# Performance work log

Measured on AMD Instinct MI355X. Metric: run time of the kernel, lower is better.

## Reference

```python
import jax, jax.numpy as jnp
import numpy as np

N = 100000      # nodes
E = 800000      # edges (avg degree 8)
F_IN = 512      # num_features
H = 256         # 2 * embedding_size
D_OUT = 128     # embedding_size


def setup_inputs() -> dict:
    key = jax.random.key(0)
    ks = jax.random.split(key, 5)
    x = jax.random.normal(ks[0], (N, F_IN), dtype=jnp.float32)
    edge_index = jax.random.randint(ks[1], (2, E), 0, N, dtype=jnp.int64)
    W1 = jax.random.normal(ks[2], (F_IN, H), dtype=jnp.float32) * (1.0 / np.sqrt(F_IN))
    b1 = jnp.zeros((H,), dtype=jnp.float32)
    W2 = jax.random.normal(ks[3], (H, D_OUT), dtype=jnp.float32) * (1.0 / np.sqrt(H))
    b2 = jnp.zeros((D_OUT,), dtype=jnp.float32)
    return {"x": x, "edge_index": edge_index, "W1": W1, "b1": b1, "W2": W2, "b2": b2}


def _gcn_conv(x, edge_index, W, b):
    # PyG GCNConv: add self-loops, symmetric deg^-1/2 normalization,
    # linear transform, scatter-add aggregation at destination nodes.
    n = x.shape[0]
    loop = jnp.arange(n, dtype=edge_index.dtype)
    src = jnp.concatenate([edge_index[0], loop])  # source j
    dst = jnp.concatenate([edge_index[1], loop])  # target i
    h = x @ W                                      # [N, F_out]
    deg = jax.ops.segment_sum(jnp.ones_like(dst, dtype=h.dtype), dst, num_segments=n)
    dinv = jnp.where(deg > 0, jax.lax.rsqrt(deg), 0.0)
    norm = dinv[src] * dinv[dst]                   # [E + N]
    msg = h[src] * norm[:, None]                   # gather + scale
    out = jax.ops.segment_sum(msg, dst, num_segments=n)
    return out + b


def reference(x, edge_index, W1, b1, W2, b2):
    h = jax.nn.relu(_gcn_conv(x, edge_index, W1, b1))
    # F.dropout with training=False is identity (eval mode)
    return _gcn_conv(h, edge_index, W2, b2)
```

## Files before the change

kernel.cpp:

```cpp
#include <hip/hip_runtime.h>


typedef float   f32x4  __attribute__((ext_vector_type(4)));
typedef float   f32x2  __attribute__((ext_vector_type(2)));
typedef __bf16  bf16x8 __attribute__((ext_vector_type(8)));
typedef __bf16  bf16x4 __attribute__((ext_vector_type(4)));
typedef __bf16  bf16x2 __attribute__((ext_vector_type(2)));

#define NN 100000
#define EE 800000
#define FIN 512
#define HID 256
#define DOUT 128

__global__ void k_count(const int* __restrict__ dst, int E, int* __restrict__ cnt) {
    int e = blockIdx.x * 256 + threadIdx.x;
    if (e < E) atomicAdd(&cnt[dst[e]], 1);
}

__global__ void k_scan1(const int* __restrict__ cnt, int* __restrict__ off,
                        int* __restrict__ sums, int n) {
    __shared__ int s[1024];
    int i = blockIdx.x * 1024 + threadIdx.x;
    int v = (i < n) ? cnt[i] : 0;
    s[threadIdx.x] = v;
    __syncthreads();
    for (int d = 1; d < 1024; d <<= 1) {
        int t = (threadIdx.x >= d) ? s[threadIdx.x - d] : 0;
        __syncthreads();
        s[threadIdx.x] += t;
        __syncthreads();
    }
    if (i < n) off[i] = s[threadIdx.x] - v;
    if (threadIdx.x == 1023) sums[blockIdx.x] = s[1023];
}

__global__ void k_scan2(int* __restrict__ sums, int nb) {
    __shared__ int s[128];
    int t = threadIdx.x;
    int v = (t < nb) ? sums[t] : 0;
    s[t] = v;
    __syncthreads();
    for (int d = 1; d < 128; d <<= 1) {
        int u = (t >= d) ? s[t - d] : 0;
        __syncthreads();
        s[t] += u;
        __syncthreads();
    }
    if (t < nb) sums[t] = s[t] - v;
}

__global__ void k_scan_fix(int* __restrict__ off, const int* __restrict__ sums,
                           const int* __restrict__ cnt, float* __restrict__ dinv, int n) {
    int i = blockIdx.x * 256 + threadIdx.x;
    if (i < n) {
        off[i] += sums[i >> 10];
        dinv[i] = rsqrtf((float)(cnt[i] + 1));
    }
}

__global__ void k_fill(const int* __restrict__ src, const int* __restrict__ dst, int E,
                       const int* __restrict__ off, int* __restrict__ cur,
                       int* __restrict__ csr) {
    int e = blockIdx.x * 256 + threadIdx.x;
    if (e < E) {
        int d = dst[e];
        int p = atomicAdd(&cur[d], 1);
        csr[off[d] + p] = src[e];
    }
}

__global__ void k_prep_w(const float* __restrict__ W1, const float* __restrict__ W2,
                         __bf16* __restrict__ W1t, __bf16* __restrict__ W2t) {
    int id = blockIdx.x * 256 + threadIdx.x;
    if (id < FIN * HID) {
        int k = id >> 8, n = id & 255;
        W1t[n * FIN + k] = (__bf16)W1[id];
    }
    int id2 = id - FIN * HID;
    if (id2 >= 0 && id2 < HID * DOUT) {
        int k = id2 >> 7, n = id2 & 127;
        W2t[n * HID + k] = (__bf16)W2[id2];
    }
}

template <int WAVES_N, bool AF32, int KTOT>
__global__ __launch_bounds__(128 * WAVES_N) void k_gemm(
    const void* __restrict__ Asrc, const __bf16* __restrict__ Bt,
    const float* __restrict__ dinv, __bf16* __restrict__ out, int M) {
    constexpr int BN  = WAVES_N * 64;
    constexpr int LDA = 40;
    __shared__ __bf16 A_lds[128 * LDA];
    __shared__ __bf16 B_lds[BN * LDA];

    const int tid = threadIdx.x;
    const int l = tid & 63, wid = tid >> 6;
    const int wm = wid & 1, wn = wid >> 1;
    const int bm = blockIdx.x;
    const int r15 = l & 15, hi = l >> 4;

    f32x4 acc[4][4] = {};

    for (int kb = 0; kb < KTOT / 32; ++kb) {
        __syncthreads();
        if constexpr (AF32) {
            int row = tid >> 2, seg = tid & 3;
            long rg = (long)bm * 128 + row;
            if (rg >= M) rg = M - 1;
            const float* ap = (const float*)Asrc + rg * (long)KTOT + kb * 32 + seg * 8;
            f32x4 x0 = *(const f32x4*)ap;
            f32x4 x1 = *(const f32x4*)(ap + 4);
            bf16x8 w;
            w[0] = (__bf16)x0[0]; w[1] = (__bf16)x0[1]; w[2] = (__bf16)x0[2]; w[3] = (__bf16)x0[3];
            w[4] = (__bf16)x1[0]; w[5] = (__bf16)x1[1]; w[6] = (__bf16)x1[2]; w[7] = (__bf16)x1[3];
            *(bf16x8*)&A_lds[row * LDA + seg * 8] = w;
        } else {
            int row = tid >> 1, seg = tid & 1;
            long rg = (long)bm * 128 + row;
            if (rg >= M) rg = M - 1;
            const __bf16* ap = (const __bf16*)Asrc + rg * (long)KTOT + kb * 32 + seg * 16;
            bf16x8 u0 = *(const bf16x8*)ap;
            bf16x8 u1 = *(const bf16x8*)(ap + 8);
            *(bf16x8*)&A_lds[row * LDA + seg * 16]     = u0;
            *(bf16x8*)&A_lds[row * LDA + seg * 16 + 8] = u1;
        }
        {
            int n = tid >> 1, seg = tid & 1;
            const __bf16* bp = Bt + (long)n * KTOT + kb * 32 + seg * 16;
            bf16x8 u0 = *(const bf16x8*)bp;
            bf16x8 u1 = *(const bf16x8*)(bp + 8);
            *(bf16x8*)&B_lds[n * LDA + seg * 16]     = u0;
            *(bf16x8*)&B_lds[n * LDA + seg * 16 + 8] = u1;
        }
        __syncthreads();

        bf16x8 af[4], bfr[4];
#pragma unroll
        for (int m = 0; m < 4; m++)
            af[m] = *(const bf16x8*)&A_lds[(wm * 64 + m * 16 + r15) * LDA + hi * 8];
#pragma unroll
        for (int n = 0; n < 4; n++)
            bfr[n] = *(const bf16x8*)&B_lds[(wn * 64 + n * 16 + r15) * LDA + hi * 8];
#pragma unroll
        for (int m = 0; m < 4; m++)
#pragma unroll
            for (int n = 0; n < 4; n++)
                acc[m][n] = __builtin_amdgcn_mfma_f32_16x16x32_bf16(bfr[n], af[m], acc[m][n], 0, 0, 0);
    }

#pragma unroll
    for (int m = 0; m < 4; m++) {
        long rg = (long)bm * 128 + wm * 64 + m * 16 + r15;
        if (rg >= M) continue;
        float di = dinv[rg];
#pragma unroll
        for (int n = 0; n < 4; n++) {
            bf16x4 o;
            o[0] = (__bf16)(acc[m][n][0] * di);
            o[1] = (__bf16)(acc[m][n][1] * di);
            o[2] = (__bf16)(acc[m][n][2] * di);
            o[3] = (__bf16)(acc[m][n][3] * di);
            int c = wn * 64 + n * 16 + hi * 4;
            *(bf16x4*)(out + rg * (long)BN + c) = o;
        }
    }
}

__global__ void k_agg1(const __bf16* __restrict__ g1, const int* __restrict__ csr,
                       const int* __restrict__ off, const int* __restrict__ cnt,
                       const float* __restrict__ dinv, const float* __restrict__ b1,
                       __bf16* __restrict__ z1, int n) {
    int node = blockIdx.x * 4 + (threadIdx.x >> 6);
    if (node >= n) return;
    int l = threadIdx.x & 63;
    bf16x4 v = *(const bf16x4*)(g1 + (size_t)node * HID + l * 4);
    float a0 = (float)v[0], a1 = (float)v[1], a2 = (float)v[2], a3 = (float)v[3];
    int s0 = off[node], e0 = s0 + cnt[node];
    for (int e = s0; e < e0; ++e) {
        int s = csr[e];
        bf16x4 u = *(const bf16x4*)(g1 + (size_t)s * HID + l * 4);
        a0 += (float)u[0]; a1 += (float)u[1]; a2 += (float)u[2]; a3 += (float)u[3];
    }
    float di = dinv[node];
    f32x4 b = *(const f32x4*)(b1 + l * 4);
    bf16x4 o;
    o[0] = (__bf16)fmaxf(a0 * di + b[0], 0.f);
    o[1] = (__bf16)fmaxf(a1 * di + b[1], 0.f);
    o[2] = (__bf16)fmaxf(a2 * di + b[2], 0.f);
    o[3] = (__bf16)fmaxf(a3 * di + b[3], 0.f);
    *(bf16x4*)(z1 + (size_t)node * HID + l * 4) = o;
}

__global__ void k_agg2(const __bf16* __restrict__ g2, const int* __restrict__ csr,
                       const int* __restrict__ off, const int* __restrict__ cnt,
                       const float* __restrict__ dinv, const float* __restrict__ b2,
                       float* __restrict__ out, int n) {
    int node = blockIdx.x * 4 + (threadIdx.x >> 6);
    if (node >= n) return;
    int l = threadIdx.x & 63;
    bf16x2 v = *(const bf16x2*)(g2 + (size_t)node * DOUT + l * 2);
    float a0 = (float)v[0], a1 = (float)v[1];
    int s0 = off[node], e0 = s0 + cnt[node];
    for (int e = s0; e < e0; ++e) {
        int s = csr[e];
        bf16x2 u = *(const bf16x2*)(g2 + (size_t)s * DOUT + l * 2);
        a0 += (float)u[0]; a1 += (float)u[1];
    }
    float di = dinv[node];
    f32x2 b = *(const f32x2*)(b2 + l * 2);
    f32x2 o;
    o[0] = a0 * di + b[0];
    o[1] = a1 * di + b[1];
    *(f32x2*)(out + (size_t)node * DOUT + l * 2) = o;
}

extern "C" void kernel_launch(void* const* d_in, const int* in_sizes, int n_in,
                              void* d_out, int out_size, void* d_ws, size_t ws_size,
                              hipStream_t stream) {
    const float* x  = (const float*)d_in[0];
    const int*   ei = (const int*)d_in[1];
    const float* W1 = (const float*)d_in[2];
    const float* b1 = (const float*)d_in[3];
    const float* W2 = (const float*)d_in[4];
    const float* b2 = (const float*)d_in[5];
    float* out = (float*)d_out;

    const int N = in_sizes[0] / FIN;
    const int E = in_sizes[1] / 2;
    const int* srcA = ei;
    const int* dstA = ei + E;

    uint8_t* w = (uint8_t*)d_ws;
    auto take = [&](size_t bytes) { uint8_t* p = w; w += (bytes + 255) & ~(size_t)255; return p; };
    int*    cnt  = (int*)take((size_t)N * 4);
    int*    cur  = (int*)take((size_t)N * 4);
    int*    off  = (int*)take((size_t)N * 4);
    float*  dinv = (float*)take((size_t)N * 4);
    int*    sums = (int*)take(4096);
    int*    csr  = (int*)take((size_t)E * 4);
    __bf16* W1t  = (__bf16*)take((size_t)FIN * HID * 2);
    __bf16* W2t  = (__bf16*)take((size_t)HID * DOUT * 2);
    __bf16* g1   = (__bf16*)take((size_t)N * HID * 2);
    __bf16* z1   = (__bf16*)take((size_t)N * HID * 2);
    __bf16* g2   = (__bf16*)take((size_t)N * DOUT * 2);

    hipMemsetAsync(cnt, 0, (size_t)N * 4, stream);
    hipMemsetAsync(cur, 0, (size_t)N * 4, stream);
    k_count<<<(E + 255) / 256, 256, 0, stream>>>(dstA, E, cnt);
    int nb = (N + 1023) / 1024;
    k_scan1<<<nb, 1024, 0, stream>>>(cnt, off, sums, N);
    k_scan2<<<1, 128, 0, stream>>>(sums, nb);
    k_scan_fix<<<(N + 255) / 256, 256, 0, stream>>>(off, sums, cnt, dinv, N);
    k_fill<<<(E + 255) / 256, 256, 0, stream>>>(srcA, dstA, E, off, cur, csr);

    k_prep_w<<<(FIN * HID + HID * DOUT + 255) / 256, 256, 0, stream>>>(W1, W2, W1t, W2t);

    const int gm = (N + 127) / 128;

    k_gemm<4, true, FIN><<<gm, 512, 0, stream>>>(x, W1t, dinv, g1, N);
    k_agg1<<<(N + 3) / 4, 256, 0, stream>>>(g1, csr, off, cnt, dinv, b1, z1, N);

    k_gemm<2, false, HID><<<gm, 256, 0, stream>>>(z1, W2t, dinv, g2, N);
    k_agg2<<<(N + 3) / 4, 256, 0, stream>>>(g2, csr, off, cnt, dinv, b2, out, N);
}
```

Measured before the change: 644.9 us.

## Double-buffer GEMM tiles with direct global-to-LDS loads and unroll aggregation gathers

Both GEMMs become double-buffered. The next K-tile is loaded through global_load_lds, the direct global-to-LDS path, while MFMAs run on the current tile. GEMM1 now uses 4 waves, each computing a 64x128 sub-tile, and drops the padded LDS stride. The aggregation kernels unroll the neighbour loop by 4 with two accumulators so more gathers are in flight. The unpadded 32-element LDS rows may cause bank conflicts, and the larger accumulator tile raises register pressure.

```diff
diff --git a/kernel.cpp b/kernel.cpp
--- a/kernel.cpp
+++ b/kernel.cpp
@@ -7,11 +7,14 @@
 typedef __bf16  bf16x4 __attribute__((ext_vector_type(4)));
 typedef __bf16  bf16x2 __attribute__((ext_vector_type(2)));
 
-#define NN 100000
-#define EE 800000
 #define FIN 512
 #define HID 256
 #define DOUT 128
+
+__device__ __forceinline__ void gload16(const void* g, void* l) {
+    __builtin_amdgcn_global_load_lds((const __attribute__((address_space(1))) void*)g,
+                                     (__attribute__((address_space(3))) void*)l, 16, 0, 0);
+}
 
 __global__ void k_count(const int* __restrict__ dst, int E, int* __restrict__ cnt) {
     int e = blockIdx.x * 256 + threadIdx.x;
@@ -84,84 +87,185 @@
     }
 }
 
-template <int WAVES_N, bool AF32, int KTOT>
-__global__ __launch_bounds__(128 * WAVES_N) void k_gemm(
-    const void* __restrict__ Asrc, const __bf16* __restrict__ Bt,
-    const float* __restrict__ dinv, __bf16* __restrict__ out, int M) {
-    constexpr int BN  = WAVES_N * 64;
-    constexpr int LDA = 40;
-    __shared__ __bf16 A_lds[128 * LDA];
-    __shared__ __bf16 B_lds[BN * LDA];
+__global__ __launch_bounds__(256, 2) void k_gemm1(
+    const float* __restrict__ x, const __bf16* __restrict__ Bt,
+    const float* __restrict__ dinv, __bf16* __restrict__ g1, int M) {
+    __shared__ __bf16 Albuf[2][128 * 32];
+    __shared__ __bf16 Blbuf[2][256 * 32];
 
     const int tid = threadIdx.x;
     const int l = tid & 63, wid = tid >> 6;
     const int wm = wid & 1, wn = wid >> 1;
-    const int bm = blockIdx.x;
     const int r15 = l & 15, hi = l >> 4;
-
-    f32x4 acc[4][4] = {};
-
-    for (int kb = 0; kb < KTOT / 32; ++kb) {
-        __syncthreads();
-        if constexpr (AF32) {
-            int row = tid >> 2, seg = tid & 3;
-            long rg = (long)bm * 128 + row;
-            if (rg >= M) rg = M - 1;
-            const float* ap = (const float*)Asrc + rg * (long)KTOT + kb * 32 + seg * 8;
-            f32x4 x0 = *(const f32x4*)ap;
-            f32x4 x1 = *(const f32x4*)(ap + 4);
-            bf16x8 w;
-            w[0] = (__bf16)x0[0]; w[1] = (__bf16)x0[1]; w[2] = (__bf16)x0[2]; w[3] = (__bf16)x0[3];
-            w[4] = (__bf16)x1[0]; w[5] = (__bf16)x1[1]; w[6] = (__bf16)x1[2]; w[7] = (__bf16)x1[3];
-            *(bf16x8*)&A_lds[row * LDA + seg * 8] = w;
-        } else {
-            int row = tid >> 1, seg = tid & 1;
-            long rg = (long)bm * 128 + row;
-            if (rg >= M) rg = M - 1;
-            const __bf16* ap = (const __bf16*)Asrc + rg * (long)KTOT + kb * 32 + seg * 16;
-            bf16x8 u0 = *(const bf16x8*)ap;
-            bf16x8 u1 = *(const bf16x8*)(ap + 8);
-            *(bf16x8*)&A_lds[row * LDA + seg * 16]     = u0;
-            *(bf16x8*)&A_lds[row * LDA + seg * 16 + 8] = u1;
-        }
-        {
-            int n = tid >> 1, seg = tid & 1;
-            const __bf16* bp = Bt + (long)n * KTOT + kb * 32 + seg * 16;
-            bf16x8 u0 = *(const bf16x8*)bp;
-            bf16x8 u1 = *(const bf16x8*)(bp + 8);
-            *(bf16x8*)&B_lds[n * LDA + seg * 16]     = u0;
-            *(bf16x8*)&B_lds[n * LDA + seg * 16 + 8] = u1;
-        }
-        __syncthreads();
-
-        bf16x8 af[4], bfr[4];
-#pragma unroll
-        for (int m = 0; m < 4; m++)
-            af[m] = *(const bf16x8*)&A_lds[(wm * 64 + m * 16 + r15) * LDA + hi * 8];
-#pragma unroll
-        for (int n = 0; n < 4; n++)
-            bfr[n] = *(const bf16x8*)&B_lds[(wn * 64 + n * 16 + r15) * LDA + hi * 8];
-#pragma unroll
-        for (int m = 0; m < 4; m++)
-#pragma unroll
-            for (int n = 0; n < 4; n++)
+    const long bm = blockIdx.x;
+
+    const int arow = tid >> 1, aseg = tid & 1;
+    long ag = bm * 128 + arow;
+    if (ag >= M) ag = M - 1;
+    const float* aptr = x + ag * (long)FIN + aseg * 16;
+    const int aoff = arow * 32 + aseg * 16;
+
+    const int bo0 = wid * 4096;
+
+    f32x4 acc[4][8] = {};
+
+    auto stageB = [&](int kb, int buf) {
+#pragma unroll
+        for (int i = 0; i < 4; ++i) {
+            int ob = bo0 + i * 1024;
+            int o = ob + l * 16;
+            int n = o >> 6, cb = o & 63;
+            const char* src = (const char*)Bt + (long)n * (FIN * 2) + kb * 64 + cb;
+            gload16(src, (char*)&Blbuf[buf][0] + ob);
+        }
+    };
+
+    stageB(0, 0);
+    {
+        const f32x4* p = (const f32x4*)aptr;
+        f32x4 p0 = p[0], p1 = p[1], p2 = p[2], p3 = p[3];
+        bf16x8 w0, w1;
+#pragma unroll
+        for (int j = 0; j < 4; ++j) {
+            w0[j] = (__bf16)p0[j]; w0[j + 4] = (__bf16)p1[j];
+            w1[j] = (__bf16)p2[j]; w1[j + 4] = (__bf16)p3[j];
+        }
+        *(bf16x8*)&Albuf[0][aoff] = w0;
+        *(bf16x8*)&Albuf[0][aoff + 8] = w1;
+    }
+    __syncthreads();
+
+    int cur = 0;
+    constexpr int NT = FIN / 32;
+    for (int kb = 0; kb < NT; ++kb) {
+        const int nxt = cur ^ 1;
+        const bool pf = (kb + 1 < NT);
+        f32x4 p0, p1, p2, p3;
+        if (pf) {
+            stageB(kb + 1, nxt);
+            const f32x4* p = (const f32x4*)(aptr + (kb + 1) * 32);
+            p0 = p[0]; p1 = p[1]; p2 = p[2]; p3 = p[3];
+        }
+
+        bf16x8 af[4], bfr[8];
+#pragma unroll
+        for (int m = 0; m < 4; ++m)
+            af[m] = *(const bf16x8*)&Albuf[cur][(wm * 64 + m * 16 + r15) * 32 + hi * 8];
+#pragma unroll
+        for (int n = 0; n < 8; ++n)
+            bfr[n] = *(const bf16x8*)&Blbuf[cur][(wn * 128 + n * 16 + r15) * 32 + hi * 8];
+#pragma unroll
+        for (int m = 0; m < 4; ++m)
+#pragma unroll
+            for (int n = 0; n < 8; ++n)
                 acc[m][n] = __builtin_amdgcn_mfma_f32_16x16x32_bf16(bfr[n], af[m], acc[m][n], 0, 0, 0);
-    }
-
-#pragma unroll
-    for (int m = 0; m < 4; m++) {
-        long rg = (long)bm * 128 + wm * 64 + m * 16 + r15;
+
+        if (pf) {
+            bf16x8 w0, w1;
+#pragma unroll
+            for (int j = 0; j < 4; ++j) {
+                w0[j] = (__bf16)p0[j]; w0[j + 4] = (__bf16)p1[j];
+                w1[j] = (__bf16)p2[j]; w1[j + 4] = (__bf16)p3[j];
+            }
+            *(bf16x8*)&Albuf[nxt][aoff] = w0;
+            *(bf16x8*)&Albuf[nxt][aoff + 8] = w1;
+        }
+        __syncthreads();
+        cur = nxt;
+    }
+
+#pragma unroll
+    for (int m = 0; m < 4; ++m) {
+        long rg = bm * 128 + wm * 64 + m * 16 + r15;
         if (rg >= M) continue;
         float di = dinv[rg];
 #pragma unroll
-        for (int n = 0; n < 4; n++) {
+        for (int n = 0; n < 8; ++n) {
+            bf16x4 o;
+            o[0] = (__bf16)(acc[m][n][0] * di);
+            o[1] = (__bf16)(acc[m][n][1] * di);
+            o[2] = (__bf16)(acc[m][n][2] * di);
+            o[3] = (__bf16)(acc[m][n][3] * di);
+            int c = wn * 128 + n * 16 + hi * 4;
+            *(bf16x4*)(g1 + rg * (long)HID + c) = o;
+        }
+    }
+}
+
+__global__ __launch_bounds__(256, 3) void k_gemm2(
+    const __bf16* __restrict__ z1, const __bf16* __restrict__ Bt,
+    const float* __restrict__ dinv, __bf16* __restrict__ g2, int M) {
+    __shared__ __bf16 Albuf[2][128 * 32];
+    __shared__ __bf16 Blbuf[2][128 * 32];
+
+    const int tid = threadIdx.x;
+    const int l = tid & 63, wid = tid >> 6;
+    const int wm = wid & 1, wn = wid >> 1;
+    const int r15 = l & 15, hi = l >> 4;
+    const long bm = blockIdx.x;
+
+    f32x4 acc[4][4] = {};
+
+    auto stage = [&](int kb, int buf) {
+#pragma unroll
+        for (int i = 0; i < 2; ++i) {
+            int ob = wid * 2048 + i * 1024;
+            int o = ob + l * 16;
+            long r = bm * 128 + (o >> 6);
+            if (r >= M) r = M - 1;
+            const char* src = (const char*)z1 + r * (HID * 2) + kb * 64 + (o & 63);
+            gload16(src, (char*)&Albuf[buf][0] + ob);
+        }
+#pragma unroll
+        for (int i = 0; i < 2; ++i) {
+            int ob = wid * 2048 + i * 1024;
+            int o = ob + l * 16;
+            int n = o >> 6;
+            const char* src = (const char*)Bt + (long)n * (HID * 2) + kb * 64 + (o & 63);
+            gload16(src, (char*)&Blbuf[buf][0] + ob);
+        }
+    };
+
+    stage(0, 0);
+    __syncthreads();
+
+    int cur = 0;
+    constexpr int NT = HID / 32;
+    for (int kb = 0; kb < NT; ++kb) {
+        const int nxt = cur ^ 1;
+        if (kb + 1 < NT) stage(kb + 1, nxt);
+
+        bf16x8 af[4], bfr[4];
+#pragma unroll
+        for (int m = 0; m < 4; ++m)
+            af[m] = *(const bf16x8*)&Albuf[cur][(wm * 64 + m * 16 + r15) * 32 + hi * 8];
+#pragma unroll
+        for (int n = 0; n < 4; ++n)
+            bfr[n] = *(const bf16x8*)&Blbuf[cur][(wn * 64 + n * 16 + r15) * 32 + hi * 8];
+#pragma unroll
+        for (int m = 0; m < 4; ++m)
+#pragma unroll
+            for (int n = 0; n < 4; ++n)
+                acc[m][n] = __builtin_amdgcn_mfma_f32_16x16x32_bf16(bfr[n], af[m], acc[m][n], 0, 0, 0);
+
+        __syncthreads();
+        cur = nxt;
+    }
+
+#pragma unroll
+    for (int m = 0; m < 4; ++m) {
+        long rg = bm * 128 + wm * 64 + m * 16 + r15;
+        if (rg >= M) continue;
+        float di = dinv[rg];
+#pragma unroll
+        for (int n = 0; n < 4; ++n) {
             bf16x4 o;
             o[0] = (__bf16)(acc[m][n][0] * di);
             o[1] = (__bf16)(acc[m][n][1] * di);
             o[2] = (__bf16)(acc[m][n][2] * di);
             o[3] = (__bf16)(acc[m][n][3] * di);
             int c = wn * 64 + n * 16 + hi * 4;
-            *(bf16x4*)(out + rg * (long)BN + c) = o;
+            *(bf16x4*)(g2 + rg * (long)DOUT + c) = o;
         }
     }
 }
@@ -173,21 +277,34 @@
     int node = blockIdx.x * 4 + (threadIdx.x >> 6);
     if (node >= n) return;
     int l = threadIdx.x & 63;
-    bf16x4 v = *(const bf16x4*)(g1 + (size_t)node * HID + l * 4);
+    const __bf16* base = g1 + (size_t)l * 4;
+    bf16x4 v = *(const bf16x4*)(base + (size_t)node * HID);
     float a0 = (float)v[0], a1 = (float)v[1], a2 = (float)v[2], a3 = (float)v[3];
-    int s0 = off[node], e0 = s0 + cnt[node];
-    for (int e = s0; e < e0; ++e) {
+    float c0 = 0.f, c1 = 0.f, c2 = 0.f, c3 = 0.f;
+    int e = off[node], e0 = e + cnt[node];
+    for (; e + 3 < e0; e += 4) {
+        int sA = csr[e], sB = csr[e + 1], sC = csr[e + 2], sD = csr[e + 3];
+        bf16x4 uA = *(const bf16x4*)(base + (size_t)sA * HID);
+        bf16x4 uB = *(const bf16x4*)(base + (size_t)sB * HID);
+        bf16x4 uC = *(const bf16x4*)(base + (size_t)sC * HID);
+        bf16x4 uD = *(const bf16x4*)(base + (size_t)sD * HID);
+        a0 += (float)uA[0] + (float)uC[0]; c0 += (float)uB[0] + (float)uD[0];
+        a1 += (float)uA[1] + (float)uC[1]; c1 += (float)uB[1] + (float)uD[1];
+        a2 += (float)uA[2] + (float)uC[2]; c2 += (float)uB[2] + (float)uD[2];
+        a3 += (float)uA[3] + (float)uC[3]; c3 += (float)uB[3] + (float)uD[3];
+    }
+    for (; e < e0; ++e) {
         int s = csr[e];
-        bf16x4 u = *(const bf16x4*)(g1 + (size_t)s * HID + l * 4);
+        bf16x4 u = *(const bf16x4*)(base + (size_t)s * HID);
         a0 += (float)u[0]; a1 += (float)u[1]; a2 += (float)u[2]; a3 += (float)u[3];
     }
     float di = dinv[node];
     f32x4 b = *(const f32x4*)(b1 + l * 4);
     bf16x4 o;
-    o[0] = (__bf16)fmaxf(a0 * di + b[0], 0.f);
-    o[1] = (__bf16)fmaxf(a1 * di + b[1], 0.f);
-    o[2] = (__bf16)fmaxf(a2 * di + b[2], 0.f);
-    o[3] = (__bf16)fmaxf(a3 * di + b[3], 0.f);
+    o[0] = (__bf16)fmaxf((a0 + c0) * di + b[0], 0.f);
+    o[1] = (__bf16)fmaxf((a1 + c1) * di + b[1], 0.f);
+    o[2] = (__bf16)fmaxf((a2 + c2) * di + b[2], 0.f);
+    o[3] = (__bf16)fmaxf((a3 + c3) * di + b[3], 0.f);
     *(bf16x4*)(z1 + (size_t)node * HID + l * 4) = o;
 }
 
@@ -198,19 +315,30 @@
     int node = blockIdx.x * 4 + (threadIdx.x >> 6);
     if (node >= n) return;
     int l = threadIdx.x & 63;
-    bf16x2 v = *(const bf16x2*)(g2 + (size_t)node * DOUT + l * 2);
+    const __bf16* base = g2 + (size_t)l * 2;
+    bf16x2 v = *(const bf16x2*)(base + (size_t)node * DOUT);
     float a0 = (float)v[0], a1 = (float)v[1];
-    int s0 = off[node], e0 = s0 + cnt[node];
-    for (int e = s0; e < e0; ++e) {
+    float c0 = 0.f, c1 = 0.f;
+    int e = off[node], e0 = e + cnt[node];
+    for (; e + 3 < e0; e += 4) {
+        int sA = csr[e], sB = csr[e + 1], sC = csr[e + 2], sD = csr[e + 3];
+        bf16x2 uA = *(const bf16x2*)(base + (size_t)sA * DOUT);
+        bf16x2 uB = *(const bf16x2*)(base + (size_t)sB * DOUT);
+        bf16x2 uC = *(const bf16x2*)(base + (size_t)sC * DOUT);
+        bf16x2 uD = *(const bf16x2*)(base + (size_t)sD * DOUT);
+        a0 += (float)uA[0] + (float)uC[0]; c0 += (float)uB[0] + (float)uD[0];
+        a1 += (float)uA[1] + (float)uC[1]; c1 += (float)uB[1] + (float)uD[1];
+    }
+    for (; e < e0; ++e) {
         int s = csr[e];
-        bf16x2 u = *(const bf16x2*)(g2 + (size_t)s * DOUT + l * 2);
+        bf16x2 u = *(const bf16x2*)(base + (size_t)s * DOUT);
         a0 += (float)u[0]; a1 += (float)u[1];
     }
     float di = dinv[node];
     f32x2 b = *(const f32x2*)(b2 + l * 2);
     f32x2 o;
-    o[0] = a0 * di + b[0];
-    o[1] = a1 * di + b[1];
+    o[0] = (a0 + c0) * di + b[0];
+    o[1] = (a1 + c1) * di + b[1];
     *(f32x2*)(out + (size_t)node * DOUT + l * 2) = o;
 }
 
@@ -257,9 +385,8 @@
 
     const int gm = (N + 127) / 128;
 
-    k_gemm<4, true, FIN><<<gm, 512, 0, stream>>>(x, W1t, dinv, g1, N);
+    k_gemm1<<<gm, 256, 0, stream>>>(x, W1t, dinv, g1, N);
     k_agg1<<<(N + 3) / 4, 256, 0, stream>>>(g1, csr, off, cnt, dinv, b1, z1, N);
-
-    k_gemm<2, false, HID><<<gm, 256, 0, stream>>>(z1, W2t, dinv, g2, N);
+    k_gemm2<<<gm, 256, 0, stream>>>(z1, W2t, dinv, g2, N);
     k_agg2<<<(N + 3) / 4, 256, 0, stream>>>(g2, csr, off, cnt, dinv, b2, out, N);
 }
```

Result: faster. 564.9 us (-12.4%).
